# Performance work log

Hardware: AMD Instinct MI355X
Metric: run time of the kernel (lower is better)

Reference implementation:

```python
import jax, jax.numpy as jnp
import numpy as np

B, T, N, D = 16, 48, 256, 64
K_HEADS = 8


def setup_inputs() -> dict:
    key = jax.random.key(0)
    ks = jax.random.split(key, 12)
    return {
        "query": jax.random.normal(ks[0], (B, T, N, D), jnp.float32),
        "key": jax.random.normal(ks[1], (B, T, N, D), jnp.float32),
        "value": jax.random.normal(ks[2], (B, T, N, D), jnp.float32),
        "key_w": jax.random.normal(ks[3], (B, T, D, D), jnp.float32) * 0.05,
        "key_b": jax.random.normal(ks[4], (B, T, D), jnp.float32) * 0.05,
        "value_w": jax.random.normal(ks[5], (B, T, D, D), jnp.float32) * 0.05,
        "value_b": jax.random.normal(ks[6], (B, T, D), jnp.float32) * 0.05,
        "proj1_w": jax.random.normal(ks[7], (D, D), jnp.float32) * 0.05,
        "proj1_b": jax.random.normal(ks[8], (D,), jnp.float32) * 0.05,
        "proj2_w": jax.random.normal(ks[9], (D, D), jnp.float32) * 0.05,
        "proj2_b": jax.random.normal(ks[10], (D,), jnp.float32) * 0.05,
        "rate": jnp.full((1,), 0.8, jnp.float32),
    }


def reference(query, key, value, key_w, key_b, value_w, value_b,
              proj1_w, proj1_b, proj2_w, proj2_b, rate):
    b, t, n, d = query.shape
    hs = d // K_HEADS
    # per-(batch,time) projections (LinearCustom)
    k = jnp.einsum('btnd,btde->btne', key, key_w) + key_b[:, :, None, :]
    v = jnp.einsum('btnd,btde->btne', value, value_w) + value_b[:, :, None, :]
    # split heads along channel dim (matches torch.split on dim -1)
    qh = query.reshape(b, t, n, K_HEADS, hs)
    kh = k.reshape(b, t, n, K_HEADS, hs)
    vh = v.reshape(b, t, n, K_HEADS, hs)
    # scores: [b, h, n, q, k]
    scores = jnp.einsum('bqnhd,bknhd->bhnqk', qh, kh) / jnp.sqrt(jnp.asarray(hs, query.dtype))
    # time decay: b_time_decays[..., i, j] = (T-1-i) + 1 = T - i (depends on query pos only)
    dec = (t - jnp.arange(t, dtype=scores.dtype))[:, None]  # [T, 1], broadcasts over key axis
    s = jax.nn.sigmoid(scores)
    denom = 1.0 + jax.nn.sigmoid(s * jax.nn.sigmoid(rate) * dec)
    att = jax.nn.softmax(jnp.tanh(s / denom), axis=-1)
    x = jnp.einsum('bhnqk,bknhd->bqnhd', att, vh).reshape(b, t, n, d)
    x = jnp.tanh(x @ proj1_w.T + proj1_b)
    return x @ proj2_w.T + proj2_b
```

## Files before the change

### kernel.cpp

```cpp
#include <hip/hip_runtime.h>


#define B_ 16
#define T_ 48
#define N_ 256
#define D_ 64

__device__ __forceinline__ float rcpf(float x) { return __builtin_amdgcn_rcpf(x); }
__device__ __forceinline__ float ex2(float x) { return __builtin_amdgcn_exp2f(x); }
#define LOG2E 1.4426950408889634f

__global__ __launch_bounds__(256) void proj_kv_kernel(
    const float* __restrict__ key, const float* __restrict__ key_w, const float* __restrict__ key_b,
    const float* __restrict__ value, const float* __restrict__ value_w, const float* __restrict__ value_b,
    float* __restrict__ k_out, float* __restrict__ v_out)
{
    const int bt = blockIdx.x;
    const int which = blockIdx.y;
    const float* __restrict__ in = (which ? value : key) + (size_t)bt * N_ * D_;
    const float* __restrict__ w  = (which ? value_w : key_w) + (size_t)bt * D_ * D_;
    const float* __restrict__ bb = (which ? value_b : key_b) + (size_t)bt * D_;
    float* __restrict__ out = (which ? v_out : k_out) + (size_t)bt * N_ * D_;

    __shared__ float Wl[D_][D_];
    __shared__ float Xl[128][68];
    __shared__ float Bl[D_];

    const int tid = threadIdx.x;
    #pragma unroll
    for (int i = tid; i < D_ * D_; i += 256) Wl[i >> 6][i & 63] = w[i];
    if (tid < D_) Bl[tid] = bb[tid];

    const int cg = tid & 7;
    const int rg = tid >> 3;

    for (int n0 = 0; n0 < N_; n0 += 128) {
        __syncthreads();
        #pragma unroll
        for (int i = tid; i < 128 * D_ / 4; i += 256) {
            const int e = i * 4;
            *(float4*)&Xl[e >> 6][e & 63] = *(const float4*)&in[(size_t)n0 * D_ + e];
        }
        __syncthreads();

        float acc[4][8];
        #pragma unroll
        for (int j = 0; j < 4; ++j)
            #pragma unroll
            for (int i = 0; i < 8; ++i) acc[j][i] = Bl[cg * 8 + i];

        #pragma unroll 8
        for (int d = 0; d < D_; ++d) {
            const float4 w0 = *(const float4*)&Wl[d][cg * 8];
            const float4 w1 = *(const float4*)&Wl[d][cg * 8 + 4];
            #pragma unroll
            for (int j = 0; j < 4; ++j) {
                const float a = Xl[rg + 32 * j][d];
                acc[j][0] += a * w0.x; acc[j][1] += a * w0.y;
                acc[j][2] += a * w0.z; acc[j][3] += a * w0.w;
                acc[j][4] += a * w1.x; acc[j][5] += a * w1.y;
                acc[j][6] += a * w1.z; acc[j][7] += a * w1.w;
            }
        }

        #pragma unroll
        for (int j = 0; j < 4; ++j) {
            const size_t row = (size_t)(n0 + rg + 32 * j);
            *(float4*)&out[row * D_ + cg * 8]     = make_float4(acc[j][0], acc[j][1], acc[j][2], acc[j][3]);
            *(float4*)&out[row * D_ + cg * 8 + 4] = make_float4(acc[j][4], acc[j][5], acc[j][6], acc[j][7]);
        }
    }
}

__global__ __launch_bounds__(256) void attn_kernel(
    const float* __restrict__ query, float* __restrict__ k_xatt, const float* __restrict__ v_in,
    const float* __restrict__ rate)
{
    const int b  = blockIdx.x >> 7;
    const int n0 = (blockIdx.x & 127) * 2;

    __shared__ float K[2][T_][68];
    __shared__ float V[2][T_][68];

    const int tid = threadIdx.x;
    #pragma unroll
    for (int i = tid; i < T_ * 16; i += 256) {
        const int t = i >> 4, d4 = (i & 15) * 4;
        const size_t g0 = ((size_t)(b * T_ + t) * N_ + n0) * D_ + d4;
        *(float4*)&K[0][t][d4] = *(const float4*)&k_xatt[g0];
        *(float4*)&V[0][t][d4] = *(const float4*)&v_in[g0];
        *(float4*)&K[1][t][d4] = *(const float4*)&k_xatt[g0 + D_];
        *(float4*)&V[1][t][d4] = *(const float4*)&v_in[g0 + D_];
    }
    const float rsig = rcpf(1.0f + ex2(-rate[0] * LOG2E));

    const int nl = tid >> 7;
    const int r  = tid & 127;
    const int qg = r >> 3;
    const int h  = r & 7;
    const int n  = n0 + nl;

    const float C1 = 0.35355339059327373f * LOG2E;
    float4 qa[3], qb[3];
    float rdn[3];
    #pragma unroll
    for (int j = 0; j < 3; ++j) {
        const int q = qg + 16 * j;
        const size_t g = ((size_t)(b * T_ + q) * N_ + n) * D_ + h * 8;
        const float4 a = *(const float4*)&query[g];
        const float4 c = *(const float4*)&query[g + 4];
        qa[j] = make_float4(-C1 * a.x, -C1 * a.y, -C1 * a.z, -C1 * a.w);
        qb[j] = make_float4(-C1 * c.x, -C1 * c.y, -C1 * c.z, -C1 * c.w);
        rdn[j] = -rsig * (float)(T_ - q) * LOG2E;
    }
    __syncthreads();

    float4 acc0[3], acc1[3];
    float ssum[3];
    #pragma unroll
    for (int j = 0; j < 3; ++j) {
        acc0[j] = make_float4(0.f, 0.f, 0.f, 0.f);
        acc1[j] = make_float4(0.f, 0.f, 0.f, 0.f);
        ssum[j] = 0.f;
    }

    #pragma unroll 2
    for (int tk = 0; tk < T_; ++tk) {
        const float4 ka = *(const float4*)&K[nl][tk][h * 8];
        const float4 kb = *(const float4*)&K[nl][tk][h * 8 + 4];
        const float4 va = *(const float4*)&V[nl][tk][h * 8];
        const float4 vb = *(const float4*)&V[nl][tk][h * 8 + 4];
        #pragma unroll
        for (int j = 0; j < 3; ++j) {
            const float dn = qa[j].x * ka.x + qa[j].y * ka.y + qa[j].z * ka.z + qa[j].w * ka.w
                           + qb[j].x * kb.x + qb[j].y * kb.y + qb[j].z * kb.z + qb[j].w * kb.w;
            const float s   = rcpf(1.0f + ex2(dn));
            const float s2  = rcpf(1.0f + ex2(s * rdn[j]));
            const float arg = s * rcpf(1.0f + s2);
            const float x2  = arg * arg;
            const float th  = arg * (15.0f + x2) * rcpf(15.0f + 6.0f * x2);
            const float e   = ex2(th * LOG2E);
            ssum[j] += e;
            acc0[j].x += e * va.x; acc0[j].y += e * va.y; acc0[j].z += e * va.z; acc0[j].w += e * va.w;
            acc1[j].x += e * vb.x; acc1[j].y += e * vb.y; acc1[j].z += e * vb.z; acc1[j].w += e * vb.w;
        }
    }

    #pragma unroll
    for (int j = 0; j < 3; ++j) {
        const float inv = rcpf(ssum[j]);
        const int q = qg + 16 * j;
        const size_t g = ((size_t)(b * T_ + q) * N_ + n) * D_ + h * 8;
        *(float4*)&k_xatt[g]     = make_float4(acc0[j].x * inv, acc0[j].y * inv, acc0[j].z * inv, acc0[j].w * inv);
        *(float4*)&k_xatt[g + 4] = make_float4(acc1[j].x * inv, acc1[j].y * inv, acc1[j].z * inv, acc1[j].w * inv);
    }
}

__global__ __launch_bounds__(256) void wtrans_kernel(
    const float* __restrict__ p1w, const float* __restrict__ p2w,
    float* __restrict__ w1t, float* __restrict__ w2t)
{
    const int i = blockIdx.x * 256 + threadIdx.x;
    if (i < D_ * D_) {
        const int d = i >> 6, c = i & 63;
        w1t[i] = p1w[c * 64 + d];
        w2t[i] = p2w[c * 64 + d];
    }
}

__global__ __launch_bounds__(256) void out_proj_kernel(
    const float* __restrict__ xatt,
    const float* __restrict__ w1t, const float* __restrict__ p1b,
    const float* __restrict__ w2t, const float* __restrict__ p2b,
    float* __restrict__ out)
{
    __shared__ float Xt[D_][132];

    const int tid = threadIdx.x;
    const size_t m0 = (size_t)blockIdx.x * 128;

    #pragma unroll
    for (int i = tid; i < 128 * 16; i += 256) {
        const int row = i >> 4, d4 = (i & 15) * 4;
        const float4 xv = *(const float4*)&xatt[(m0 + row) * D_ + d4];
        Xt[d4 + 0][row] = xv.x;
        Xt[d4 + 1][row] = xv.y;
        Xt[d4 + 2][row] = xv.z;
        Xt[d4 + 3][row] = xv.w;
    }
    __syncthreads();

    const int l  = tid & 63;
    const int c0 = __builtin_amdgcn_readfirstlane((tid >> 6) * 16);

    float a0[16], a1[16];
    #pragma unroll
    for (int c = 0; c < 16; ++c) {
        const float bv = p1b[c0 + c];
        a0[c] = bv; a1[c] = bv;
    }
    for (int d = 0; d < D_; ++d) {
        const float x0 = Xt[d][l];
        const float x1 = Xt[d][l + 64];
        const float* wr = w1t + __builtin_amdgcn_readfirstlane(d * 64 + c0);
        #pragma unroll
        for (int c = 0; c < 16; ++c) {
            const float wv = wr[c];
            a0[c] += x0 * wv;
            a1[c] += x1 * wv;
        }
    }
    #pragma unroll
    for (int c = 0; c < 16; ++c) {
        a0[c] = 1.0f - 2.0f * rcpf(ex2(a0[c] * (2.0f * LOG2E)) + 1.0f);
        a1[c] = 1.0f - 2.0f * rcpf(ex2(a1[c] * (2.0f * LOG2E)) + 1.0f);
    }
    __syncthreads();
    #pragma unroll
    for (int c = 0; c < 16; ++c) {
        Xt[c0 + c][l]      = a0[c];
        Xt[c0 + c][l + 64] = a1[c];
    }
    __syncthreads();

    float o0[16], o1[16];
    #pragma unroll
    for (int c = 0; c < 16; ++c) {
        const float bv = p2b[c0 + c];
        o0[c] = bv; o1[c] = bv;
    }
    for (int d = 0; d < D_; ++d) {
        const float x0 = Xt[d][l];
        const float x1 = Xt[d][l + 64];
        const float* wr = w2t + __builtin_amdgcn_readfirstlane(d * 64 + c0);
        #pragma unroll
        for (int c = 0; c < 16; ++c) {
            const float wv = wr[c];
            o0[c] += x0 * wv;
            o1[c] += x1 * wv;
        }
    }
    #pragma unroll
    for (int k = 0; k < 4; ++k) {
        *(float4*)&out[(m0 + l) * D_ + c0 + 4 * k]      = make_float4(o0[4*k], o0[4*k+1], o0[4*k+2], o0[4*k+3]);
        *(float4*)&out[(m0 + l + 64) * D_ + c0 + 4 * k] = make_float4(o1[4*k], o1[4*k+1], o1[4*k+2], o1[4*k+3]);
    }
}

extern "C" void kernel_launch(void* const* d_in, const int* in_sizes, int n_in,
                              void* d_out, int out_size, void* d_ws, size_t ws_size,
                              hipStream_t stream) {
    const float* query   = (const float*)d_in[0];
    const float* key     = (const float*)d_in[1];
    const float* value   = (const float*)d_in[2];
    const float* key_w   = (const float*)d_in[3];
    const float* key_b   = (const float*)d_in[4];
    const float* value_w = (const float*)d_in[5];
    const float* value_b = (const float*)d_in[6];
    const float* p1w     = (const float*)d_in[7];
    const float* p1b     = (const float*)d_in[8];
    const float* p2w     = (const float*)d_in[9];
    const float* p2b     = (const float*)d_in[10];
    const float* rate    = (const float*)d_in[11];
    float* out = (float*)d_out;

    float* kws = (float*)d_ws;
    float* vws = kws + (size_t)B_ * T_ * N_ * D_;
    float* w1t = vws;
    float* w2t = vws + D_ * D_;

    dim3 gridA(B_ * T_, 2);
    proj_kv_kernel<<<gridA, 256, 0, stream>>>(key, key_w, key_b, value, value_w, value_b, kws, vws);
    attn_kernel<<<B_ * (N_ / 2), 256, 0, stream>>>(query, kws, vws, rate);
    wtrans_kernel<<<16, 256, 0, stream>>>(p1w, p2w, w1t, w2t);
    out_proj_kernel<<<(B_ * T_ * N_) / 128, 256, 0, stream>>>(kws, w1t, p1b, w2t, p2b, out);
}
```

Before: 241.6 us.

## Retile output projection GEMMs and trim one reciprocal from attention math

The output-projection kernel moves from a transposed LDS layout with a per-thread 16-column slice and scalar weight loads to a row-major padded tile. Each thread now computes a 4-row by 8-column block using float4 loads of X and the weights, and the kernel gets a 4-blocks-per-CU occupancy hint. The attention inner loop rewrites the sigmoid-denominator step algebraically so one reciprocal per score is removed, and the key-time loop is unrolled by 4. The aim is fewer LDS and global load instructions and fewer transcendental ops, at the cost of more register pressure.

```diff
diff --git a/kernel.cpp b/kernel.cpp
--- a/kernel.cpp
+++ b/kernel.cpp
@@ -124,7 +124,7 @@
         ssum[j] = 0.f;
     }
 
-    #pragma unroll 2
+    #pragma unroll 4
     for (int tk = 0; tk < T_; ++tk) {
         const float4 ka = *(const float4*)&K[nl][tk][h * 8];
         const float4 kb = *(const float4*)&K[nl][tk][h * 8 + 4];
@@ -134,9 +134,10 @@
         for (int j = 0; j < 3; ++j) {
             const float dn = qa[j].x * ka.x + qa[j].y * ka.y + qa[j].z * ka.z + qa[j].w * ka.w
                            + qb[j].x * kb.x + qb[j].y * kb.y + qb[j].z * kb.z + qb[j].w * kb.w;
-            const float s   = rcpf(1.0f + ex2(dn));
-            const float s2  = rcpf(1.0f + ex2(s * rdn[j]));
-            const float arg = s * rcpf(1.0f + s2);
+            const float E1  = ex2(dn);
+            const float s   = rcpf(1.0f + E1);
+            const float E2  = ex2(s * rdn[j]);
+            const float arg = s * (1.0f + E2) * rcpf(2.0f + E2);
             const float x2  = arg * arg;
             const float th  = arg * (15.0f + x2) * rcpf(15.0f + 6.0f * x2);
             const float e   = ex2(th * LOG2E);
@@ -168,13 +169,13 @@
     }
 }
 
-__global__ __launch_bounds__(256) void out_proj_kernel(
+__global__ __launch_bounds__(256, 4) void out_proj_kernel(
     const float* __restrict__ xatt,
     const float* __restrict__ w1t, const float* __restrict__ p1b,
     const float* __restrict__ w2t, const float* __restrict__ p2b,
     float* __restrict__ out)
 {
-    __shared__ float Xt[D_][132];
+    __shared__ float X[128][68];
 
     const int tid = threadIdx.x;
     const size_t m0 = (size_t)blockIdx.x * 128;
@@ -182,68 +183,92 @@
     #pragma unroll
     for (int i = tid; i < 128 * 16; i += 256) {
         const int row = i >> 4, d4 = (i & 15) * 4;
-        const float4 xv = *(const float4*)&xatt[(m0 + row) * D_ + d4];
-        Xt[d4 + 0][row] = xv.x;
-        Xt[d4 + 1][row] = xv.y;
-        Xt[d4 + 2][row] = xv.z;
-        Xt[d4 + 3][row] = xv.w;
+        *(float4*)&X[row][d4] = *(const float4*)&xatt[(m0 + row) * D_ + d4];
     }
     __syncthreads();
 
-    const int l  = tid & 63;
-    const int c0 = __builtin_amdgcn_readfirstlane((tid >> 6) * 16);
-
-    float a0[16], a1[16];
-    #pragma unroll
-    for (int c = 0; c < 16; ++c) {
-        const float bv = p1b[c0 + c];
-        a0[c] = bv; a1[c] = bv;
-    }
-    for (int d = 0; d < D_; ++d) {
-        const float x0 = Xt[d][l];
-        const float x1 = Xt[d][l + 64];
-        const float* wr = w1t + __builtin_amdgcn_readfirstlane(d * 64 + c0);
-        #pragma unroll
-        for (int c = 0; c < 16; ++c) {
-            const float wv = wr[c];
-            a0[c] += x0 * wv;
-            a1[c] += x1 * wv;
-        }
-    }
-    #pragma unroll
-    for (int c = 0; c < 16; ++c) {
-        a0[c] = 1.0f - 2.0f * rcpf(ex2(a0[c] * (2.0f * LOG2E)) + 1.0f);
-        a1[c] = 1.0f - 2.0f * rcpf(ex2(a1[c] * (2.0f * LOG2E)) + 1.0f);
+    const int cg = tid & 7;
+    const int rg = tid >> 3;
+
+    float x1[4][8];
+    {
+        float acc[4][8];
+        #pragma unroll
+        for (int i = 0; i < 8; ++i) {
+            const float bv = p1b[cg * 8 + i];
+            #pragma unroll
+            for (int j = 0; j < 4; ++j) acc[j][i] = bv;
+        }
+        #pragma unroll 4
+        for (int d0 = 0; d0 < D_; d0 += 4) {
+            float4 w0[4], w1[4];
+            #pragma unroll
+            for (int dd = 0; dd < 4; ++dd) {
+                w0[dd] = *(const float4*)&w1t[(d0 + dd) * 64 + cg * 8];
+                w1[dd] = *(const float4*)&w1t[(d0 + dd) * 64 + cg * 8 + 4];
+            }
+            #pragma unroll
+            for (int j = 0; j < 4; ++j) {
+                const float4 xv = *(const float4*)&X[rg + 32 * j][d0];
+                acc[j][0] += xv.x * w0[0].x + xv.y * w0[1].x + xv.z * w0[2].x + xv.w * w0[3].x;
+                acc[j][1] += xv.x * w0[0].y + xv.y * w0[1].y + xv.z * w0[2].y + xv.w * w0[3].y;
+                acc[j][2] += xv.x * w0[0].z + xv.y * w0[1].z + xv.z * w0[2].z + xv.w * w0[3].z;
+                acc[j][3] += xv.x * w0[0].w + xv.y * w0[1].w + xv.z * w0[2].w + xv.w * w0[3].w;
+                acc[j][4] += xv.x * w1[0].x + xv.y * w1[1].x + xv.z * w1[2].x + xv.w * w1[3].x;
+                acc[j][5] += xv.x * w1[0].y + xv.y * w1[1].y + xv.z * w1[2].y + xv.w * w1[3].y;
+                acc[j][6] += xv.x * w1[0].z + xv.y * w1[1].z + xv.z * w1[2].z + xv.w * w1[3].z;
+                acc[j][7] += xv.x * w1[0].w + xv.y * w1[1].w + xv.z * w1[2].w + xv.w * w1[3].w;
+            }
+        }
+        #pragma unroll
+        for (int j = 0; j < 4; ++j)
+            #pragma unroll
+            for (int i = 0; i < 8; ++i)
+                x1[j][i] = 1.0f - 2.0f * rcpf(ex2(acc[j][i] * (2.0f * LOG2E)) + 1.0f);
     }
     __syncthreads();
     #pragma unroll
-    for (int c = 0; c < 16; ++c) {
-        Xt[c0 + c][l]      = a0[c];
-        Xt[c0 + c][l + 64] = a1[c];
+    for (int j = 0; j < 4; ++j) {
+        *(float4*)&X[rg + 32 * j][cg * 8]     = make_float4(x1[j][0], x1[j][1], x1[j][2], x1[j][3]);
+        *(float4*)&X[rg + 32 * j][cg * 8 + 4] = make_float4(x1[j][4], x1[j][5], x1[j][6], x1[j][7]);
     }
     __syncthreads();
 
-    float o0[16], o1[16];
-    #pragma unroll
-    for (int c = 0; c < 16; ++c) {
-        const float bv = p2b[c0 + c];
-        o0[c] = bv; o1[c] = bv;
-    }
-    for (int d = 0; d < D_; ++d) {
-        const float x0 = Xt[d][l];
-        const float x1 = Xt[d][l + 64];
-        const float* wr = w2t + __builtin_amdgcn_readfirstlane(d * 64 + c0);
-        #pragma unroll
-        for (int c = 0; c < 16; ++c) {
-            const float wv = wr[c];
-            o0[c] += x0 * wv;
-            o1[c] += x1 * wv;
-        }
-    }
-    #pragma unroll
-    for (int k = 0; k < 4; ++k) {
-        *(float4*)&out[(m0 + l) * D_ + c0 + 4 * k]      = make_float4(o0[4*k], o0[4*k+1], o0[4*k+2], o0[4*k+3]);
-        *(float4*)&out[(m0 + l + 64) * D_ + c0 + 4 * k] = make_float4(o1[4*k], o1[4*k+1], o1[4*k+2], o1[4*k+3]);
+    {
+        float acc[4][8];
+        #pragma unroll
+        for (int i = 0; i < 8; ++i) {
+            const float bv = p2b[cg * 8 + i];
+            #pragma unroll
+            for (int j = 0; j < 4; ++j) acc[j][i] = bv;
+        }
+        #pragma unroll 4
+        for (int d0 = 0; d0 < D_; d0 += 4) {
+            float4 w0[4], w1[4];
+            #pragma unroll
+            for (int dd = 0; dd < 4; ++dd) {
+                w0[dd] = *(const float4*)&w2t[(d0 + dd) * 64 + cg * 8];
+                w1[dd] = *(const float4*)&w2t[(d0 + dd) * 64 + cg * 8 + 4];
+            }
+            #pragma unroll
+            for (int j = 0; j < 4; ++j) {
+                const float4 xv = *(const float4*)&X[rg + 32 * j][d0];
+                acc[j][0] += xv.x * w0[0].x + xv.y * w0[1].x + xv.z * w0[2].x + xv.w * w0[3].x;
+                acc[j][1] += xv.x * w0[0].y + xv.y * w0[1].y + xv.z * w0[2].y + xv.w * w0[3].y;
+                acc[j][2] += xv.x * w0[0].z + xv.y * w0[1].z + xv.z * w0[2].z + xv.w * w0[3].z;
+                acc[j][3] += xv.x * w0[0].w + xv.y * w0[1].w + xv.z * w0[2].w + xv.w * w0[3].w;
+                acc[j][4] += xv.x * w1[0].x + xv.y * w1[1].x + xv.z * w1[2].x + xv.w * w1[3].x;
+                acc[j][5] += xv.x * w1[0].y + xv.y * w1[1].y + xv.z * w1[2].y + xv.w * w1[3].y;
+                acc[j][6] += xv.x * w1[0].z + xv.y * w1[1].z + xv.z * w1[2].z + xv.w * w1[3].z;
+                acc[j][7] += xv.x * w1[0].w + xv.y * w1[1].w + xv.z * w1[2].w + xv.w * w1[3].w;
+            }
+        }
+        #pragma unroll
+        for (int j = 0; j < 4; ++j) {
+            const size_t og = (m0 + rg + 32 * j) * D_ + cg * 8;
+            *(float4*)&out[og]     = make_float4(acc[j][0], acc[j][1], acc[j][2], acc[j][3]);
+            *(float4*)&out[og + 4] = make_float4(acc[j][4], acc[j][5], acc[j][6], acc[j][7]);
+        }
     }
 }
 
```

Measured after the change: 233.3 us. 3.4% less time.
